# Kernel optimization log

Measured on AMD Instinct MI355X. Metric: run time of the kernel, lower is better.

Reference implementation:

```python
import jax, jax.numpy as jnp
import numpy as np

IN_F, OUT_F = 1024, 1024
GRID_SIZE, SPLINE_ORDER = 5, 3
BATCH = 4096
GRID_LO, GRID_HI = -1.0, 1.0


def _make_grid():
    h = (GRID_HI - GRID_LO) / GRID_SIZE
    g = jnp.arange(-SPLINE_ORDER, GRID_SIZE + SPLINE_ORDER + 1, dtype=jnp.float32) * h + GRID_LO  # [12]
    return jnp.broadcast_to(g, (IN_F, g.shape[0]))  # [in, 12]


def setup_inputs() -> dict:
    key = jax.random.key(0)
    k1, k2, k3 = jax.random.split(key, 3)
    x = jax.random.normal(k1, (BATCH, IN_F), dtype=jnp.float32)
    base_weight = jax.random.normal(k2, (OUT_F, IN_F), dtype=jnp.float32) * (1.0 / np.sqrt(IN_F))
    spline_weight = jax.random.normal(k3, (OUT_F, IN_F, GRID_SIZE + SPLINE_ORDER), dtype=jnp.float32) * 0.1
    spline_scaler = jnp.ones((OUT_F, IN_F), dtype=jnp.float32)
    grid = _make_grid()
    return {"x": x, "base_weight": base_weight, "spline_weight": spline_weight,
            "spline_scaler": spline_scaler, "grid": grid}


def b_splines(x, grid):
    # x: [B, in], grid: [in, 12] -> bases: [B, in, grid_size+spline_order]
    xe = x[..., None]  # [B, in, 1]
    bases = ((xe >= grid[:, :-1]) & (xe < grid[:, 1:])).astype(x.dtype)  # [B, in, 11]
    for k in range(1, SPLINE_ORDER + 1):
        t0 = grid[:, :-(k + 1)]
        t1 = grid[:, k:-1]
        t2 = grid[:, k + 1:]
        t3 = grid[:, 1:-k]
        bases = ((xe - t0) / (t1 - t0 + 1e-8) * bases[..., :-1]
                 + (t2 - xe) / (t2 - t3 + 1e-8) * bases[..., 1:])
    return bases


def reference(x, base_weight, spline_weight, spline_scaler, grid):
    base_output = jax.nn.silu(x) @ base_weight.T  # [B, out]
    spline_basis = b_splines(x, grid)             # [B, in, 8]
    spline_output = jnp.einsum('bij,oij,oi->bo', spline_basis, spline_weight, spline_scaler)
    return base_output + spline_output
```

## Files before the change

### kernel.cpp

```cpp
#include <hip/hip_runtime.h>
#include <hip/hip_bf16.h>
#include <stdint.h>
#include <stddef.h>

#define IN_F     1024
#define OUT_F    1024
#define BATCH    4096
#define NSPLINE  8
#define KDIM     (IN_F * 9)
#define GRIDPTS  12

typedef __bf16 bf16;
typedef __bf16 bf16x2 __attribute__((ext_vector_type(2)));
typedef __bf16 bf16x8 __attribute__((ext_vector_type(8)));
typedef float  f32x4  __attribute__((ext_vector_type(4)));

#define NB_BUILD (BATCH * IN_F / 512)
#define NB_PACK  (OUT_F * IN_F / 512)

__global__ __launch_bounds__(256) void prep(const float* __restrict__ x,
                                            const float* __restrict__ grid,
                                            const float* __restrict__ bw,
                                            const float* __restrict__ sw,
                                            const float* __restrict__ sc,
                                            bf16* __restrict__ A,
                                            bf16* __restrict__ W)
{
    __shared__ float g[GRIDPTS];
    __shared__ float rec[33];

    if (blockIdx.x < NB_BUILD) {
        if (threadIdx.x < GRIDPTS) g[threadIdx.x] = grid[threadIdx.x];
        __syncthreads();
        if (threadIdx.x < 33) {
            const int k = threadIdx.x / 11 + 1;
            const int j = threadIdx.x % 11;
            if (j + k <= 11) rec[threadIdx.x] = 1.0f / (g[j + k] - g[j] + 1e-8f);
        }
        __syncthreads();

        const int idx2 = blockIdx.x * 256 + threadIdx.x;
        const int e0 = idx2 * 2;
        const int b = e0 >> 10;
        const int i = e0 & 1023;
        const float2 xv2 = *(const float2*)(x + e0);

        float bs[2][11];
#pragma unroll
        for (int u = 0; u < 2; ++u) {
            const float xv = u ? xv2.y : xv2.x;
#pragma unroll
            for (int j = 0; j < 11; ++j)
                bs[u][j] = (xv >= g[j] && xv < g[j + 1]) ? 1.0f : 0.0f;
#pragma unroll
            for (int k = 1; k <= 3; ++k) {
                const float* rk = &rec[(k - 1) * 11];
#pragma unroll
                for (int j = 0; j < 10; ++j) {
                    if (j <= 10 - k) {
                        bs[u][j] = (xv - g[j]) * rk[j] * bs[u][j]
                                 + (g[j + k + 1] - xv) * rk[j + 1] * bs[u][j + 1];
                    }
                }
            }
        }

        const float s0 = xv2.x / (1.0f + __expf(-xv2.x));
        const float s1 = xv2.y / (1.0f + __expf(-xv2.y));

        bf16* rowp = A + (size_t)b * KDIM;
        *(bf16x2*)&rowp[i] = (bf16x2){(bf16)s0, (bf16)s1};
#pragma unroll
        for (int j = 0; j < NSPLINE; ++j)
            *(bf16x2*)&rowp[(size_t)(j + 1) * IN_F + i] =
                (bf16x2){(bf16)bs[0][j], (bf16)bs[1][j]};
    } else {
        const int idx2 = (blockIdx.x - NB_BUILD) * 256 + threadIdx.x;
        const int e0 = idx2 * 2;
        const int i = e0 & 1023;
        const float2 s2 = *(const float2*)(sc + e0);
        const float2 bw2 = *(const float2*)(bw + e0);

        bf16* rowp = W + (size_t)(e0 >> 10) * KDIM;
        *(bf16x2*)&rowp[i] = (bf16x2){(bf16)bw2.x, (bf16)bw2.y};

        const float4* swv = (const float4*)(sw + (size_t)e0 * NSPLINE);
        const float4 a0 = swv[0], a1 = swv[1];
        const float4 c0 = swv[2], c1 = swv[3];
        float w0[NSPLINE] = {a0.x, a0.y, a0.z, a0.w, a1.x, a1.y, a1.z, a1.w};
        float w1[NSPLINE] = {c0.x, c0.y, c0.z, c0.w, c1.x, c1.y, c1.z, c1.w};
#pragma unroll
        for (int j = 0; j < NSPLINE; ++j)
            *(bf16x2*)&rowp[(size_t)(j + 1) * IN_F + i] =
                (bf16x2){(bf16)(w0[j] * s2.x), (bf16)(w1[j] * s2.y)};
    }
}

#define BM8 256
#define BN8 128
#define BK8 32
#define SPLIT 4
#define KLEN (KDIM / SPLIT)
#define NT8  (KLEN / BK8)

#define GLOAD_LDS16(gp, lp)                                                          \
    __builtin_amdgcn_global_load_lds((const __attribute__((address_space(1))) void*)(gp), \
                                     (__attribute__((address_space(3))) void*)(lp), 16, 0, 0)

__global__ __launch_bounds__(512, 4) void gemm8(const bf16* __restrict__ A,
                                                const bf16* __restrict__ B,
                                                float* __restrict__ C)
{
    __shared__ bf16 lds[24576];

    const int tid  = threadIdx.x;
    const int wave = tid >> 6;
    const int lane = tid & 63;

    const int nwg  = gridDim.x;
    const int q    = nwg >> 3;
    const int wgid = (blockIdx.x & 7) * q + (blockIdx.x >> 3);
    const int nxy  = (BATCH / BM8) * (OUT_F / BN8);
    const int z    = wgid / nxy;
    const int rem  = wgid - z * nxy;
    const int by   = rem >> 4;
    const int bx   = rem & 15;

    const int bm   = bx * BM8;
    const int bcol = by * BN8;
    const int kBase = z * KLEN;
    C += (size_t)z * BATCH * OUT_F;

    const int wr = (wave >> 2) * 128;
    const int wc = (wave & 3) * 32;

    f32x4 acc[8][2] = {};

    const int srow = tid >> 2;
    const int sch  = (((tid & 3) ^ ((tid >> 3) & 3))) * 8;
    const bf16* pA0 = A + (size_t)(bm + srow) * KDIM + kBase + sch;
    const bf16* pA1 = pA0 + (size_t)128 * KDIM;
    const bf16* pB0 = B + (size_t)(bcol + srow) * KDIM + kBase + sch;
    bf16* ldswA = lds + wave * 512;
    bf16* ldswB = lds + 16384 + wave * 512;

    auto stageA = [&](int t, int s) {
        const int kof = t * BK8;
        GLOAD_LDS16(pA0 + kof, ldswA + s * 8192);
        GLOAD_LDS16(pA1 + kof, ldswA + s * 8192 + 4096);
    };
    auto stageB = [&](int t, int s) {
        GLOAD_LDS16(pB0 + t * BK8, ldswB + s * 4096);
    };

    stageA(0, 0);
    stageB(0, 0);
    asm volatile("s_waitcnt vmcnt(0)" ::: "memory");
    __builtin_amdgcn_s_barrier();

    const int rowk = lane & 15;
    const int kc   = lane >> 4;
    const int kxor = (kc ^ ((rowk >> 1) & 3)) * 8;

#define LDSA(s, row) (*(const bf16x8*)&lds[(s) * 8192 + (row) * 32 + kxor])
#define LDSB(s, row) (*(const bf16x8*)&lds[16384 + (s) * 4096 + (row) * 32 + kxor])

    for (int t = 0; t < NT8; ++t) {
        const int p = t & 1;
        bf16x8 a[4], b[2], a2[4];

        if (t + 1 < NT8) stageA(t + 1, 1 - p);
#pragma unroll
        for (int m = 0; m < 4; ++m) a[m] = LDSA(p, wr + m * 16 + rowk);
#pragma unroll
        for (int n = 0; n < 2; ++n) b[n] = LDSB(p, wc + n * 16 + rowk);
        if (t + 1 < NT8) stageB(t + 1, 1 - p);
#pragma unroll
        for (int m = 0; m < 4; ++m) a2[m] = LDSA(p, wr + 64 + m * 16 + rowk);
        __builtin_amdgcn_sched_barrier(0);

        __builtin_amdgcn_s_setprio(1);
#pragma unroll
        for (int m = 0; m < 4; ++m)
#pragma unroll
            for (int n = 0; n < 2; ++n)
                acc[m][n] = __builtin_amdgcn_mfma_f32_16x16x32_bf16(a[m], b[n], acc[m][n], 0, 0, 0);
#pragma unroll
        for (int m = 0; m < 4; ++m)
#pragma unroll
            for (int n = 0; n < 2; ++n)
                acc[4 + m][n] = __builtin_amdgcn_mfma_f32_16x16x32_bf16(a2[m], b[n], acc[4 + m][n], 0, 0, 0);
        __builtin_amdgcn_s_setprio(0);

        if (t + 1 < NT8) asm volatile("s_waitcnt vmcnt(0)" ::: "memory");
        __builtin_amdgcn_s_barrier();
    }
#undef LDSA
#undef LDSB

    const int ccol = lane & 15;
    const int crow = (lane >> 4) * 4;
#pragma unroll
    for (int mf = 0; mf < 8; ++mf) {
#pragma unroll
        for (int nf = 0; nf < 2; ++nf) {
            float* cp = C + (size_t)(bm + wr + mf * 16 + crow) * OUT_F + (bcol + wc + nf * 16 + ccol);
#pragma unroll
            for (int r = 0; r < 4; ++r)
                cp[(size_t)r * OUT_F] = acc[mf][nf][r];
        }
    }
}

__global__ __launch_bounds__(256) void reduce_partials(const float4* __restrict__ P,
                                                       float4* __restrict__ out,
                                                       int n4)
{
    const int stride = gridDim.x * 256;
    for (int i = blockIdx.x * 256 + threadIdx.x; i < n4; i += stride) {
        float4 s = P[i];
#pragma unroll
        for (int p = 1; p < SPLIT; ++p) {
            const float4 q = P[(size_t)p * n4 + i];
            s.x += q.x; s.y += q.y; s.z += q.z; s.w += q.w;
        }
        out[i] = s;
    }
}

extern "C" void kernel_launch(void* const* d_in, const int* in_sizes, int n_in,
                              void* d_out, int out_size, void* d_ws, size_t ws_size,
                              hipStream_t stream)
{
    const float* x  = (const float*)d_in[0];
    const float* bw = (const float*)d_in[1];
    const float* sw = (const float*)d_in[2];
    const float* sc = (const float*)d_in[3];
    const float* gr = (const float*)d_in[4];
    float* out = (float*)d_out;

    bf16* A = (bf16*)d_ws;
    bf16* W = A + (size_t)BATCH * KDIM;
    float* parts = (float*)(W + (size_t)OUT_F * KDIM);

    prep<<<NB_BUILD + NB_PACK, 256, 0, stream>>>(x, gr, bw, sw, sc, A, W);

    const int nblk = (BATCH / BM8) * (OUT_F / BN8) * SPLIT;
    gemm8<<<nblk, 512, 0, stream>>>(A, W, parts);

    const int n4 = BATCH * OUT_F / 4;
    reduce_partials<<<2048, 256, 0, stream>>>((const float4*)parts, (float4*)out, n4);
}
```

Baseline: 127.7 us.

## Triple-buffer LDS tiles in split-K GEMM with prefetch distance two

Moves the bf16 GEMM main loop from double to triple buffering of A/B tiles in LDS. Tiles are prefetched two steps ahead, and the wait uses vmcnt(3) instead of vmcnt(0), so one tile's global-to-LDS loads can stay in flight across the barrier. The loop is unrolled by three through a TILE macro so buffer indices are constants. The aim is to hide global load latency, at the cost of raising LDS use from 48KB to 72KB per block, which may reduce how many blocks fit per CU.

```diff
diff --git a/kernel.cpp b/kernel.cpp
--- a/kernel.cpp
+++ b/kernel.cpp
@@ -111,7 +111,7 @@
                                                 const bf16* __restrict__ B,
                                                 float* __restrict__ C)
 {
-    __shared__ bf16 lds[24576];
+    __shared__ bf16 lds[36864];
 
     const int tid  = threadIdx.x;
     const int wave = tid >> 6;
@@ -142,20 +142,15 @@
     const bf16* pA1 = pA0 + (size_t)128 * KDIM;
     const bf16* pB0 = B + (size_t)(bcol + srow) * KDIM + kBase + sch;
     bf16* ldswA = lds + wave * 512;
-    bf16* ldswB = lds + 16384 + wave * 512;
-
-    auto stageA = [&](int t, int s) {
-        const int kof = t * BK8;
-        GLOAD_LDS16(pA0 + kof, ldswA + s * 8192);
-        GLOAD_LDS16(pA1 + kof, ldswA + s * 8192 + 4096);
-    };
-    auto stageB = [&](int t, int s) {
-        GLOAD_LDS16(pB0 + t * BK8, ldswB + s * 4096);
-    };
-
-    stageA(0, 0);
-    stageB(0, 0);
-    asm volatile("s_waitcnt vmcnt(0)" ::: "memory");
+    bf16* ldswB = lds + 24576 + wave * 512;
+
+    GLOAD_LDS16(pA0, ldswA);
+    GLOAD_LDS16(pA1, ldswA + 4096);
+    GLOAD_LDS16(pB0, ldswB);
+    GLOAD_LDS16(pA0 + BK8, ldswA + 8192);
+    GLOAD_LDS16(pA1 + BK8, ldswA + 8192 + 4096);
+    GLOAD_LDS16(pB0 + BK8, ldswB + 4096);
+    asm volatile("s_waitcnt vmcnt(3)" ::: "memory");
     __builtin_amdgcn_s_barrier();
 
     const int rowk = lane & 15;
@@ -163,38 +158,39 @@
     const int kxor = (kc ^ ((rowk >> 1) & 3)) * 8;
 
 #define LDSA(s, row) (*(const bf16x8*)&lds[(s) * 8192 + (row) * 32 + kxor])
-#define LDSB(s, row) (*(const bf16x8*)&lds[16384 + (s) * 4096 + (row) * 32 + kxor])
-
-    for (int t = 0; t < NT8; ++t) {
-        const int p = t & 1;
-        bf16x8 a[4], b[2], a2[4];
-
-        if (t + 1 < NT8) stageA(t + 1, 1 - p);
-#pragma unroll
-        for (int m = 0; m < 4; ++m) a[m] = LDSA(p, wr + m * 16 + rowk);
-#pragma unroll
-        for (int n = 0; n < 2; ++n) b[n] = LDSB(p, wc + n * 16 + rowk);
-        if (t + 1 < NT8) stageB(t + 1, 1 - p);
-#pragma unroll
-        for (int m = 0; m < 4; ++m) a2[m] = LDSA(p, wr + 64 + m * 16 + rowk);
-        __builtin_amdgcn_sched_barrier(0);
-
-        __builtin_amdgcn_s_setprio(1);
-#pragma unroll
-        for (int m = 0; m < 4; ++m)
-#pragma unroll
-            for (int n = 0; n < 2; ++n)
-                acc[m][n] = __builtin_amdgcn_mfma_f32_16x16x32_bf16(a[m], b[n], acc[m][n], 0, 0, 0);
-#pragma unroll
-        for (int m = 0; m < 4; ++m)
-#pragma unroll
-            for (int n = 0; n < 2; ++n)
-                acc[4 + m][n] = __builtin_amdgcn_mfma_f32_16x16x32_bf16(a2[m], b[n], acc[4 + m][n], 0, 0, 0);
-        __builtin_amdgcn_s_setprio(0);
-
-        if (t + 1 < NT8) asm volatile("s_waitcnt vmcnt(0)" ::: "memory");
-        __builtin_amdgcn_s_barrier();
-    }
+#define LDSB(s, row) (*(const bf16x8*)&lds[24576 + (s) * 4096 + (row) * 32 + kxor])
+
+#define TILE(T, S, SN)                                                          \
+  {                                                                             \
+    bf16x8 a[4], b[2], a2[4];                                                   \
+    if ((T) + 2 < NT8) {                                                        \
+        GLOAD_LDS16(pA0 + ((T) + 2) * BK8, ldswA + (SN) * 8192);                \
+        GLOAD_LDS16(pA1 + ((T) + 2) * BK8, ldswA + (SN) * 8192 + 4096);         \
+    }                                                                           \
+    _Pragma("unroll") for (int m = 0; m < 4; ++m) a[m] = LDSA(S, wr + m * 16 + rowk); \
+    _Pragma("unroll") for (int n = 0; n < 2; ++n) b[n] = LDSB(S, wc + n * 16 + rowk); \
+    if ((T) + 2 < NT8) GLOAD_LDS16(pB0 + ((T) + 2) * BK8, ldswB + (SN) * 4096); \
+    _Pragma("unroll") for (int m = 0; m < 4; ++m) a2[m] = LDSA(S, wr + 64 + m * 16 + rowk); \
+    __builtin_amdgcn_sched_barrier(0);                                          \
+    __builtin_amdgcn_s_setprio(1);                                              \
+    _Pragma("unroll") for (int m = 0; m < 4; ++m)                               \
+    _Pragma("unroll") for (int n = 0; n < 2; ++n)                               \
+        acc[m][n] = __builtin_amdgcn_mfma_f32_16x16x32_bf16(a[m], b[n], acc[m][n], 0, 0, 0); \
+    _Pragma("unroll") for (int m = 0; m < 4; ++m)                               \
+    _Pragma("unroll") for (int n = 0; n < 2; ++n)                               \
+        acc[4 + m][n] = __builtin_amdgcn_mfma_f32_16x16x32_bf16(a2[m], b[n], acc[4 + m][n], 0, 0, 0); \
+    __builtin_amdgcn_s_setprio(0);                                              \
+    if ((T) < NT8 - 3)       asm volatile("s_waitcnt vmcnt(3)" ::: "memory");   \
+    else if ((T) == NT8 - 3) asm volatile("s_waitcnt vmcnt(0)" ::: "memory");   \
+    __builtin_amdgcn_s_barrier();                                               \
+  }
+
+    for (int tt = 0; tt < NT8; tt += 3) {
+        TILE(tt,     0, 2)
+        TILE(tt + 1, 1, 0)
+        TILE(tt + 2, 2, 1)
+    }
+#undef TILE
 #undef LDSA
 #undef LDSB
 
```

Measured after the change: 129.4 us. No clear change (+1.3%).
